# Optimization experiments

Measured on AMD Instinct MI355X. Metric: run time of the kernel, lower is better.

## Reference

```python
import jax, jax.numpy as jnp
import numpy as np

T, C, H, N = 1024, 2048, 32, 64
D_LORA, D_G = 64, 128

def _ln(x, w, b, eps=1e-5):
    m = x.mean(-1, keepdims=True)
    v = ((x - m) ** 2).mean(-1, keepdims=True)
    return (x - m) * jax.lax.rsqrt(v + eps) * w + b

def setup_inputs():
    key = jax.random.key(0)
    ks = iter(jax.random.split(key, 48))
    rn = lambda shape, s=1.0: jax.random.normal(next(ks), shape, dtype=jnp.float32) * s
    return {
        "x": rn((T, C)),
        "x_prev_att": rn((C,)),
        "vk_state": rn((H, N, N), 0.1),
        "x_prev_ffn": rn((C,)),
        "v_first": rn((T, C)),
        "ln1_w": jnp.ones((C,), jnp.float32), "ln1_b": jnp.zeros((C,), jnp.float32),
        "x_r": rn((C,), 0.1), "x_w": rn((C,), 0.1), "x_k": rn((C,), 0.1),
        "x_v": rn((C,), 0.1), "x_a": rn((C,), 0.1), "x_g": rn((C,), 0.1),
        "w0": rn((C,), 0.1), "w1": rn((C, D_LORA), 0.02), "w2": rn((D_LORA, C), 0.02),
        "a0": rn((C,), 0.1), "a1": rn((C, D_LORA), 0.02), "a2": rn((D_LORA, C), 0.02),
        "v0": rn((C,), 0.1), "v1": rn((C, D_LORA), 0.02), "v2": rn((D_LORA, C), 0.02),
        "g1": rn((C, D_G), 0.02), "g2": rn((D_G, C), 0.02),
        "k_k": rn((C,), 0.1), "k_a": rn((C,), 0.1), "r_k": rn((C,), 0.1),
        "R_": rn((C, C), 0.02), "K_": rn((C, C), 0.02),
        "V_": rn((C, C), 0.02), "O_": rn((C, C), 0.02),
        "lnx_w": jnp.ones((C,), jnp.float32), "lnx_b": jnp.zeros((C,), jnp.float32),
        "ln2_w": jnp.ones((C,), jnp.float32), "ln2_b": jnp.zeros((C,), jnp.float32),
        "ffn_x_k": rn((C,), 0.1),
        "ffn_K": rn((C, 4 * C), 0.02), "ffn_V": rn((4 * C, C), 0.02),
    }

def reference(x, x_prev_att, vk_state, x_prev_ffn, v_first, ln1_w, ln1_b,
              x_r, x_w, x_k, x_v, x_a, x_g, w0, w1, w2, a0, a1, a2,
              v0, v1, v2, g1, g2, k_k, k_a, r_k, R_, K_, V_, O_,
              lnx_w, lnx_b, ln2_w, ln2_b, ffn_x_k, ffn_K, ffn_V):
    # ---- TMix: RWKV-7 time mixing (layer_id = 1, so v_first blend is active) ----
    xln = _ln(x, ln1_w, ln1_b)                                  # [T, C]
    dx = jnp.concatenate([x_prev_att[None, :], xln[:-1]], axis=0) - xln  # token shift
    xr, xw, xk, xv, xa, xg = (xln + dx * m for m in (x_r, x_w, x_k, x_v, x_a, x_g))
    r = xr @ R_
    w = jnp.tanh(xw @ w1) @ w2
    k = xk @ K_
    v = xv @ V_
    a = jax.nn.sigmoid(a0 + (xa @ a1) @ a2)
    g = jax.nn.sigmoid(xg @ g1) @ g2
    kk = (k * k_k).reshape(T, H, N)
    kk = kk / jnp.maximum(jnp.linalg.norm(kk, axis=-1, keepdims=True), 1e-12)  # L2 normalize per head
    k = k * (1.0 + (a - 1.0) * k_a)
    v = v + (v_first - v) * jax.nn.sigmoid(v0 + (xv @ v1) @ v2)  # layer_id != 0 path
    w = jnp.exp(-0.606531 * jax.nn.sigmoid(w0 + w))               # per-channel decay in (0,1)
    rh, kh, vh = r.reshape(T, H, N), k.reshape(T, H, N), v.reshape(T, H, N)
    ah, wh = a.reshape(T, H, N), w.reshape(T, H, N)

    def step(state, inp):
        # state: [H, N, N]; generalized delta rule: state*w + state@(-kk)(kk*a)^T + v k^T
        w_t, kk_t, a_t, k_t, v_t, r_t = inp
        ab = jnp.einsum('hi,hj->hij', -kk_t, kk_t * a_t)
        vk = jnp.einsum('hi,hj->hij', v_t, k_t)
        state = state * w_t[:, None, :] + jnp.einsum('hij,hjk->hik', state, ab) + vk
        return state, jnp.einsum('hij,hj->hi', state, r_t)

    vk_state, outs = jax.lax.scan(step, vk_state, (wh, kk, ah, kh, vh, rh))  # outs: [T, H, N]
    # group norm over H groups, eps = 0.00064, affine per-channel
    m = outs.mean(-1, keepdims=True)
    var = ((outs - m) ** 2).mean(-1, keepdims=True)
    gn = ((outs - m) * jax.lax.rsqrt(var + 0.00064)).reshape(T, C) * lnx_w + lnx_b
    bonus = ((r * k * r_k).reshape(T, H, N).sum(-1, keepdims=True) * vh).reshape(T, C)
    x = x + ((gn + bonus) * g) @ O_
    # ---- CMix: gated squared-ReLU MLP ----
    xln2 = _ln(x, ln2_w, ln2_b)
    dx2 = jnp.concatenate([x_prev_ffn[None, :], xln2[:-1]], axis=0) - xln2
    kf = jax.nn.relu((xln2 + dx2 * ffn_x_k) @ ffn_K) ** 2
    x = x + kf @ ffn_V
    return x
```

## Files before the change

### kernel.cpp

```cpp
#include <hip/hip_runtime.h>
#include <hip/hip_bf16.h>


#define T_ 1024
#define C_ 2048
#define H_ 32
#define NH 64

typedef __attribute__((ext_vector_type(8))) short short8v;
typedef __attribute__((ext_vector_type(4))) float f32x4;

__device__ __forceinline__ float bf2f(unsigned short u) {
  union { float f; unsigned int i; } c; c.i = ((unsigned int)u) << 16; return c.f;
}
__device__ __forceinline__ unsigned short f2bf(float f) {
  union { float f; unsigned int i; } c; c.f = f;
  unsigned int x = c.i;
  return (unsigned short)((x + 0x7fffu + ((x >> 16) & 1u)) >> 16);
}
__device__ __forceinline__ float sigm(float x) { return 1.f / (1.f + __expf(-x)); }

__device__ __forceinline__ void load8bf(const unsigned short* p, float* o) {
  union { int4 v; unsigned short u[8]; } c;
  c.v = *(const int4*)p;
#pragma unroll
  for (int i = 0; i < 8; ++i) o[i] = bf2f(c.u[i]);
}
__device__ __forceinline__ void store8bf(unsigned short* p, const float* o) {
  union { int4 v; unsigned short u[8]; } c;
#pragma unroll
  for (int i = 0; i < 8; ++i) c.u[i] = f2bf(o[i]);
  *(int4*)p = c.v;
}
__device__ __forceinline__ void load8f(const float* p, float* o) {
  float4 a = ((const float4*)p)[0], b = ((const float4*)p)[1];
  o[0] = a.x; o[1] = a.y; o[2] = a.z; o[3] = a.w;
  o[4] = b.x; o[5] = b.y; o[6] = b.z; o[7] = b.w;
}
__device__ __forceinline__ void load4f(const float* p, float* o) {
  float4 a = *(const float4*)p;
  o[0] = a.x; o[1] = a.y; o[2] = a.z; o[3] = a.w;
}

#define GLD16(g, l)                                                        \
  __builtin_amdgcn_global_load_lds(                                        \
      (const __attribute__((address_space(1))) void*)(g),                  \
      (__attribute__((address_space(3))) void*)(l), 16, 0, 0)

__global__ __launch_bounds__(256) void ln_kernel(const float* __restrict__ x,
                                                 const float* __restrict__ w,
                                                 const float* __restrict__ b,
                                                 unsigned short* __restrict__ out) {
  int t = blockIdx.x, tid = threadIdx.x;
  const float* xr = x + (size_t)t * C_;
  float v[8];
  load8f(xr + tid * 8, v);
  float s = 0.f, q = 0.f;
#pragma unroll
  for (int i = 0; i < 8; ++i) { s += v[i]; q += v[i] * v[i]; }
  for (int m = 1; m < 64; m <<= 1) { s += __shfl_xor(s, m); q += __shfl_xor(q, m); }
  __shared__ float rs[4], rq[4];
  if ((tid & 63) == 0) { rs[tid >> 6] = s; rq[tid >> 6] = q; }
  __syncthreads();
  s = rs[0] + rs[1] + rs[2] + rs[3];
  q = rq[0] + rq[1] + rq[2] + rq[3];
  float mean = s * (1.f / C_);
  float var = q * (1.f / C_) - mean * mean;
  float rstd = rsqrtf(var + 1e-5f);
  int c = tid * 8;
  float o[8];
#pragma unroll
  for (int i = 0; i < 8; ++i) o[i] = (v[i] - mean) * rstd * w[c + i] + b[c + i];
  store8bf(out + (size_t)t * C_ + c, o);
}

__global__ __launch_bounds__(256) void mix6_kernel(
    const unsigned short* __restrict__ xln, const float* __restrict__ xprev,
    const float* __restrict__ mr, const float* __restrict__ mw,
    const float* __restrict__ mk, const float* __restrict__ mv,
    const float* __restrict__ ma, const float* __restrict__ mg,
    unsigned short* xr, unsigned short* xw, unsigned short* xk,
    unsigned short* xv, unsigned short* xa, unsigned short* xg) {
  int t = blockIdx.x, tid = threadIdx.x, c = tid * 8;
  float cur[8], prv[8];
  load8bf(xln + (size_t)t * C_ + c, cur);
  if (t == 0) load8f(xprev + c, prv);
  else load8bf(xln + (size_t)(t - 1) * C_ + c, prv);
  float cf[8], o[8];
  const float* coefs[6] = {mr, mw, mk, mv, ma, mg};
  unsigned short* outs6[6] = {xr, xw, xk, xv, xa, xg};
#pragma unroll
  for (int a = 0; a < 6; ++a) {
    load8f(coefs[a] + c, cf);
#pragma unroll
    for (int i = 0; i < 8; ++i) o[i] = cur[i] + (prv[i] - cur[i]) * cf[i];
    store8bf(outs6[a] + (size_t)t * C_ + c, o);
  }
}

__global__ __launch_bounds__(256) void mix1_kernel(
    const unsigned short* __restrict__ xln, const float* __restrict__ xprev,
    const float* __restrict__ coef, unsigned short* __restrict__ o) {
  int t = blockIdx.x, tid = threadIdx.x, c = tid * 8;
  float cur[8], prv[8], cf[8], o8[8];
  load8bf(xln + (size_t)t * C_ + c, cur);
  if (t == 0) load8f(xprev + c, prv);
  else load8bf(xln + (size_t)(t - 1) * C_ + c, prv);
  load8f(coef + c, cf);
#pragma unroll
  for (int i = 0; i < 8; ++i) o8[i] = cur[i] + (prv[i] - cur[i]) * cf[i];
  store8bf(o + (size_t)t * C_ + c, o8);
}

__global__ __launch_bounds__(256) void transpose_kernel(
    const float* in0, const float* in1, const float* in2,
    unsigned short* o0, unsigned short* o1, unsigned short* o2,
    int R, int Cc) {
  const float* in = blockIdx.z == 0 ? in0 : (blockIdx.z == 1 ? in1 : in2);
  unsigned short* out = blockIdx.z == 0 ? o0 : (blockIdx.z == 1 ? o1 : o2);
  __shared__ __align__(16) unsigned short tile[64][80];
  int c0 = blockIdx.x * 64, r0 = blockIdx.y * 64;
  int rr = threadIdx.x >> 4, cq = threadIdx.x & 15;
#pragma unroll
  for (int i = 0; i < 4; ++i) {
    int r = rr + i * 16;
    float4 v = *(const float4*)(in + (size_t)(r0 + r) * Cc + c0 + cq * 4);
    tile[cq * 4 + 0][r] = f2bf(v.x);
    tile[cq * 4 + 1][r] = f2bf(v.y);
    tile[cq * 4 + 2][r] = f2bf(v.z);
    tile[cq * 4 + 3][r] = f2bf(v.w);
  }
  __syncthreads();
  int cr = threadIdx.x >> 2, rg = threadIdx.x & 3;
  int4 w0 = *(const int4*)&tile[cr][rg * 16];
  int4 w1 = *(const int4*)&tile[cr][rg * 16 + 8];
  unsigned short* op = out + (size_t)(c0 + cr) * R + r0 + rg * 16;
  *(int4*)op = w0;
  *(int4*)(op + 8) = w1;
}

template <int EPI>
__global__ __launch_bounds__(256) void gemm2_kernel(
    const unsigned short* A0, const unsigned short* A1, const unsigned short* A2,
    const unsigned short* B0, const unsigned short* B1, const unsigned short* B2,
    void* C0, void* C1, void* C2, const float* __restrict__ addsrc,
    int M, int K, int N) {
  int z = blockIdx.z;
  const unsigned short* A = z == 0 ? A0 : (z == 1 ? A1 : A2);
  const unsigned short* Bt = z == 0 ? B0 : (z == 1 ? B1 : B2);
  void* Cout = z == 0 ? C0 : (z == 1 ? C1 : C2);
  __shared__ __align__(16) unsigned short As[128 * 32];
  __shared__ __align__(16) unsigned short Bs[128 * 32];
  const int tid = threadIdx.x, lane = tid & 63, wid = tid >> 6;
  const int bm = blockIdx.y * 128, bn = blockIdx.x * 128;
  const int wr = wid >> 1, wc = wid & 1;
  const int mrow = lane & 15, krow = lane >> 4;
  f32x4 acc[4][4] = {};
  for (int kt = 0; kt < K; kt += 32) {
#pragma unroll
    for (int q = 0; q < 2; ++q) {
      int s = q * 2048 + tid * 8;
      int m = s >> 5, k = s & 31;
      GLD16(A + (size_t)(bm + m) * K + kt + k, &As[s]);
      GLD16(Bt + (size_t)(bn + m) * K + kt + k, &Bs[s]);
    }
    __syncthreads();
    short8v af[4], bfrag[4];
#pragma unroll
    for (int i = 0; i < 4; ++i)
      af[i] = *(const short8v*)&As[(wr * 64 + i * 16 + mrow) * 32 + krow * 8];
#pragma unroll
    for (int j = 0; j < 4; ++j)
      bfrag[j] = *(const short8v*)&Bs[(wc * 64 + j * 16 + mrow) * 32 + krow * 8];
#pragma unroll
    for (int i = 0; i < 4; ++i)
#pragma unroll
      for (int j = 0; j < 4; ++j)
        acc[i][j] = __builtin_amdgcn_mfma_f32_16x16x32_bf16(af[i], bfrag[j], acc[i][j], 0, 0, 0);
    __syncthreads();
  }
#pragma unroll
  for (int i = 0; i < 4; ++i)
#pragma unroll
    for (int j = 0; j < 4; ++j)
#pragma unroll
      for (int e = 0; e < 4; ++e) {
        int grow = bm + wr * 64 + i * 16 + (lane >> 4) * 4 + e;
        int gcol = bn + wc * 64 + j * 16 + (lane & 15);
        size_t off = (size_t)grow * N + gcol;
        float v = acc[i][j][e];
        if constexpr (EPI == 0) ((float*)Cout)[off] = v;
        else if constexpr (EPI == 1) ((float*)Cout)[off] = addsrc[off] + v;
        else { float r = v > 0.f ? v : 0.f; ((unsigned short*)Cout)[off] = f2bf(r * r); }
      }
}

__global__ __launch_bounds__(256) void gemm2ks_kernel(
    const unsigned short* __restrict__ A, const unsigned short* __restrict__ Bt,
    float* __restrict__ P, int M, int KH, int Ktot, int N) {
  int kz = blockIdx.z;
  const size_t kbase = (size_t)kz * KH;
  __shared__ __align__(16) unsigned short As[128 * 32];
  __shared__ __align__(16) unsigned short Bs[128 * 32];
  const int tid = threadIdx.x, lane = tid & 63, wid = tid >> 6;
  const int bm = blockIdx.y * 128, bn = blockIdx.x * 128;
  const int wr = wid >> 1, wc = wid & 1;
  const int mrow = lane & 15, krow = lane >> 4;
  f32x4 acc[4][4] = {};
  for (int kt = 0; kt < KH; kt += 32) {
#pragma unroll
    for (int q = 0; q < 2; ++q) {
      int s = q * 2048 + tid * 8;
      int m = s >> 5, k = s & 31;
      GLD16(A + (size_t)(bm + m) * Ktot + kbase + kt + k, &As[s]);
      GLD16(Bt + (size_t)(bn + m) * Ktot + kbase + kt + k, &Bs[s]);
    }
    __syncthreads();
    short8v af[4], bfrag[4];
#pragma unroll
    for (int i = 0; i < 4; ++i)
      af[i] = *(const short8v*)&As[(wr * 64 + i * 16 + mrow) * 32 + krow * 8];
#pragma unroll
    for (int j = 0; j < 4; ++j)
      bfrag[j] = *(const short8v*)&Bs[(wc * 64 + j * 16 + mrow) * 32 + krow * 8];
#pragma unroll
    for (int i = 0; i < 4; ++i)
#pragma unroll
      for (int j = 0; j < 4; ++j)
        acc[i][j] = __builtin_amdgcn_mfma_f32_16x16x32_bf16(af[i], bfrag[j], acc[i][j], 0, 0, 0);
    __syncthreads();
  }
  float* Pz = P + (size_t)kz * M * N;
#pragma unroll
  for (int i = 0; i < 4; ++i)
#pragma unroll
    for (int j = 0; j < 4; ++j)
#pragma unroll
      for (int e = 0; e < 4; ++e) {
        int grow = bm + wr * 64 + i * 16 + (lane >> 4) * 4 + e;
        int gcol = bn + wc * 64 + j * 16 + (lane & 15);
        Pz[(size_t)grow * N + gcol] = acc[i][j][e];
      }
}

__global__ __launch_bounds__(256) void gemm2ks3_kernel(
    const unsigned short* A0, const unsigned short* A1, const unsigned short* A2,
    const unsigned short* B0, const unsigned short* B1, const unsigned short* B2,
    float* __restrict__ P, int M, int KH, int Ktot, int N) {
  int z = blockIdx.z;
  int batch = z % 3, kz = z / 3;
  const unsigned short* A = batch == 0 ? A0 : (batch == 1 ? A1 : A2);
  const unsigned short* Bt = batch == 0 ? B0 : (batch == 1 ? B1 : B2);
  const size_t kbase = (size_t)kz * KH;
  __shared__ __align__(16) unsigned short As[128 * 32];
  __shared__ __align__(16) unsigned short Bs[128 * 32];
  const int tid = threadIdx.x, lane = tid & 63, wid = tid >> 6;
  const int bm = blockIdx.y * 128, bn = blockIdx.x * 128;
  const int wr = wid >> 1, wc = wid & 1;
  const int mrow = lane & 15, krow = lane >> 4;
  f32x4 acc[4][4] = {};
  for (int kt = 0; kt < KH; kt += 32) {
#pragma unroll
    for (int q = 0; q < 2; ++q) {
      int s = q * 2048 + tid * 8;
      int m = s >> 5, k = s & 31;
      GLD16(A + (size_t)(bm + m) * Ktot + kbase + kt + k, &As[s]);
      GLD16(Bt + (size_t)(bn + m) * Ktot + kbase + kt + k, &Bs[s]);
    }
    __syncthreads();
    short8v af[4], bfrag[4];
#pragma unroll
    for (int i = 0; i < 4; ++i)
      af[i] = *(const short8v*)&As[(wr * 64 + i * 16 + mrow) * 32 + krow * 8];
#pragma unroll
    for (int j = 0; j < 4; ++j)
      bfrag[j] = *(const short8v*)&Bs[(wc * 64 + j * 16 + mrow) * 32 + krow * 8];
#pragma unroll
    for (int i = 0; i < 4; ++i)
#pragma unroll
      for (int j = 0; j < 4; ++j)
        acc[i][j] = __builtin_amdgcn_mfma_f32_16x16x32_bf16(af[i], bfrag[j], acc[i][j], 0, 0, 0);
    __syncthreads();
  }
  float* Pz = P + (size_t)z * M * N;
#pragma unroll
  for (int i = 0; i < 4; ++i)
#pragma unroll
    for (int j = 0; j < 4; ++j)
#pragma unroll
      for (int e = 0; e < 4; ++e) {
        int grow = bm + wr * 64 + i * 16 + (lane >> 4) * 4 + e;
        int gcol = bn + wc * 64 + j * 16 + (lane & 15);
        Pz[(size_t)grow * N + gcol] = acc[i][j][e];
      }
}

__global__ __launch_bounds__(256) void addsk3_kernel(float* __restrict__ q) {
  size_t i = ((size_t)blockIdx.x * 256 + threadIdx.x) * 4;
  float4 a = *(const float4*)(q + i);
  float4 b = *(const float4*)(q + i + 3ull * T_ * C_);
  float4 r;
  r.x = a.x + b.x; r.y = a.y + b.y; r.z = a.z + b.z; r.w = a.w + b.w;
  *(float4*)(q + i) = r;
}

__global__ __launch_bounds__(256) void add5_kernel(
    const float* __restrict__ a, const float* __restrict__ p,
    float* __restrict__ o) {
  size_t i = ((size_t)blockIdx.x * 256 + threadIdx.x) * 4;
  const size_t TC = (size_t)T_ * C_;
  float4 va = *(const float4*)(a + i);
  float4 v0 = *(const float4*)(p + i);
  float4 v1 = *(const float4*)(p + i + TC);
  float4 v2 = *(const float4*)(p + i + 2 * TC);
  float4 v3 = *(const float4*)(p + i + 3 * TC);
  float4 r;
  r.x = va.x + v0.x + v1.x + v2.x + v3.x;
  r.y = va.y + v0.y + v1.y + v2.y + v3.y;
  r.z = va.z + v0.z + v1.z + v2.z + v3.z;
  r.w = va.w + v0.w + v1.w + v2.w + v3.w;
  *(float4*)(o + i) = r;
}

__global__ __launch_bounds__(256) void gemm_ks3_kernel(
    const unsigned short* A0, const unsigned short* A1, const unsigned short* A2,
    const unsigned short* B0, const unsigned short* B1, const unsigned short* B2,
    float* P0, float* P1, float* P2, int K, int N) {
  int mz = blockIdx.z >> 3, kz = blockIdx.z & 7;
  const unsigned short* A = mz == 0 ? A0 : (mz == 1 ? A1 : A2);
  const unsigned short* Bt = mz == 0 ? B0 : (mz == 1 ? B1 : B2);
  float* partial = mz == 0 ? P0 : (mz == 1 ? P1 : P2);
  __shared__ __align__(16) unsigned short As[128 * 32];
  __shared__ __align__(16) unsigned short Bs[64 * 32];
  const int tid = threadIdx.x, lane = tid & 63, wid = tid >> 6;
  const int bn = blockIdx.x * 64, bm = blockIdx.y * 128;
  const int wr = wid >> 1, wc = wid & 1;
  const int mrow = lane & 15, krow = lane >> 4;
  f32x4 acc[4][2] = {};
  for (int kt = kz * 256; kt < kz * 256 + 256; kt += 32) {
#pragma unroll
    for (int q = 0; q < 2; ++q) {
      int s = q * 2048 + tid * 8;
      int m = s >> 5, k = s & 31;
      GLD16(A + (size_t)(bm + m) * K + kt + k, &As[s]);
    }
    {
      int s = tid * 8;
      int n = s >> 5, k = s & 31;
      GLD16(Bt + (size_t)(bn + n) * K + kt + k, &Bs[s]);
    }
    __syncthreads();
    short8v af[4], bfrag[2];
#pragma unroll
    for (int i = 0; i < 4; ++i)
      af[i] = *(const short8v*)&As[(wr * 64 + i * 16 + mrow) * 32 + krow * 8];
#pragma unroll
    for (int j = 0; j < 2; ++j)
      bfrag[j] = *(const short8v*)&Bs[(wc * 32 + j * 16 + mrow) * 32 + krow * 8];
#pragma unroll
    for (int i = 0; i < 4; ++i)
#pragma unroll
      for (int j = 0; j < 2; ++j)
        acc[i][j] = __builtin_amdgcn_mfma_f32_16x16x32_bf16(af[i], bfrag[j], acc[i][j], 0, 0, 0);
    __syncthreads();
  }
#pragma unroll
  for (int i = 0; i < 4; ++i)
#pragma unroll
    for (int j = 0; j < 2; ++j)
#pragma unroll
      for (int e = 0; e < 4; ++e) {
        int row = bm + wr * 64 + i * 16 + (lane >> 4) * 4 + e;
        int col = bn + wc * 32 + j * 16 + (lane & 15);
        partial[((size_t)kz * 1024 + row) * N + col] = acc[i][j][e];
      }
}

__global__ __launch_bounds__(256) void gemm_ks_kernel(
    const unsigned short* __restrict__ A, const unsigned short* __restrict__ Bt,
    float* __restrict__ partial, int K, int N) {
  __shared__ __align__(16) unsigned short As[128 * 32];
  __shared__ __align__(16) unsigned short Bs[64 * 32];
  const int tid = threadIdx.x, lane = tid & 63, wid = tid >> 6;
  const int bn = blockIdx.x * 64, bm = blockIdx.y * 128, kz = blockIdx.z;
  const int wr = wid >> 1, wc = wid & 1;
  const int mrow = lane & 15, krow = lane >> 4;
  f32x4 acc[4][2] = {};
  for (int kt = kz * 256; kt < kz * 256 + 256; kt += 32) {
#pragma unroll
    for (int q = 0; q < 2; ++q) {
      int s = q * 2048 + tid * 8;
      int m = s >> 5, k = s & 31;
      GLD16(A + (size_t)(bm + m) * K + kt + k, &As[s]);
    }
    {
      int s = tid * 8;
      int n = s >> 5, k = s & 31;
      GLD16(Bt + (size_t)(bn + n) * K + kt + k, &Bs[s]);
    }
    __syncthreads();
    short8v af[4], bfrag[2];
#pragma unroll
    for (int i = 0; i < 4; ++i)
      af[i] = *(const short8v*)&As[(wr * 64 + i * 16 + mrow) * 32 + krow * 8];
#pragma unroll
    for (int j = 0; j < 2; ++j)
      bfrag[j] = *(const short8v*)&Bs[(wc * 32 + j * 16 + mrow) * 32 + krow * 8];
#pragma unroll
    for (int i = 0; i < 4; ++i)
#pragma unroll
      for (int j = 0; j < 2; ++j)
        acc[i][j] = __builtin_amdgcn_mfma_f32_16x16x32_bf16(af[i], bfrag[j], acc[i][j], 0, 0, 0);
    __syncthreads();
  }
#pragma unroll
  for (int i = 0; i < 4; ++i)
#pragma unroll
    for (int j = 0; j < 2; ++j)
#pragma unroll
      for (int e = 0; e < 4; ++e) {
        int row = bm + wr * 64 + i * 16 + (lane >> 4) * 4 + e;
        int col = bn + wc * 32 + j * 16 + (lane & 15);
        partial[((size_t)kz * 1024 + row) * N + col] = acc[i][j][e];
      }
}

__global__ __launch_bounds__(128) void lora_combine_kernel(
    const float* __restrict__ pw, const float* __restrict__ pa,
    const float* __restrict__ pv, const float* __restrict__ pg,
    unsigned short* __restrict__ hw, unsigned short* __restrict__ ha,
    unsigned short* __restrict__ hv, unsigned short* __restrict__ hg) {
  int t = blockIdx.x, which = blockIdx.y, tid = threadIdx.x;
  int Nl = (which == 3) ? 128 : 64;
  if (tid >= Nl) return;
  const float* p = which == 0 ? pw : which == 1 ? pa : which == 2 ? pv : pg;
  float s = 0.f;
#pragma unroll
  for (int kz = 0; kz < 8; ++kz) s += p[((size_t)kz * 1024 + t) * Nl + tid];
  float r = which == 0 ? tanhf(s) : (which == 3 ? sigm(s) : s);
  unsigned short* o = which == 0 ? hw : which == 1 ? ha : which == 2 ? hv : hg;
  o[t * Nl + tid] = f2bf(r);
}

__global__ __launch_bounds__(256) void post_kernel(
    const float* __restrict__ k_, const float* __restrict__ vraw,
    const float* __restrict__ r_, const float* __restrict__ wpre,
    const float* __restrict__ apre, const float* __restrict__ vpre,
    const float* __restrict__ vfirst, const float* __restrict__ w0,
    const float* __restrict__ a0, const float* __restrict__ v0_,
    const float* __restrict__ k_k, const float* __restrict__ k_a,
    float* __restrict__ scanin) {
  int t = blockIdx.x, tid = threadIdx.x;
  int c = tid * 8, h = tid >> 3, j = c & 63;
  size_t o = (size_t)t * C_ + c;
  float kv[8], vv[8], rv[8], wv[8], av[8], vp[8], vf[8];
  load8f(k_ + o, kv); load8f(vraw + o, vv); load8f(r_ + o, rv);
  load8f(wpre + o, wv); load8f(apre + o, av); load8f(vpre + o, vp);
  load8f(vfirst + o, vf);
  float ckk[8], cka[8], cw0[8], ca0[8], cv0[8];
  load8f(k_k + c, ckk); load8f(k_a + c, cka); load8f(w0 + c, cw0);
  load8f(a0 + c, ca0); load8f(v0_ + c, cv0);
  float kk[8]; float ss = 0.f;
#pragma unroll
  for (int i = 0; i < 8; ++i) { kk[i] = kv[i] * ckk[i]; ss += kk[i] * kk[i]; }
  ss += __shfl_xor(ss, 1); ss += __shfl_xor(ss, 2); ss += __shfl_xor(ss, 4);
  float rdn = 1.f / fmaxf(sqrtf(ss), 1e-12f);
  float sw[8], skn[8], scc[8], sk2[8], sv[8];
#pragma unroll
  for (int i = 0; i < 8; ++i) {
    float kkn = kk[i] * rdn;
    float a = sigm(ca0[i] + av[i]);
    skn[i] = kkn;
    scc[i] = -kkn * a;
    sk2[i] = kv[i] * (1.f + (a - 1.f) * cka[i]);
    float sg = sigm(cv0[i] + vp[i]);
    sv[i] = vv[i] + (vf[i] - vv[i]) * sg;
    sw[i] = __expf(-0.606531f * sigm(cw0[i] + wv[i]));
  }
  float* bp = scanin + ((size_t)h * T_ + t) * 384 + j;
  ((float4*)(bp + 0))[0]   = make_float4(sw[0], sw[1], sw[2], sw[3]);
  ((float4*)(bp + 4))[0]   = make_float4(sw[4], sw[5], sw[6], sw[7]);
  ((float4*)(bp + 64))[0]  = make_float4(skn[0], skn[1], skn[2], skn[3]);
  ((float4*)(bp + 68))[0]  = make_float4(skn[4], skn[5], skn[6], skn[7]);
  ((float4*)(bp + 128))[0] = make_float4(scc[0], scc[1], scc[2], scc[3]);
  ((float4*)(bp + 132))[0] = make_float4(scc[4], scc[5], scc[6], scc[7]);
  ((float4*)(bp + 192))[0] = make_float4(sk2[0], sk2[1], sk2[2], sk2[3]);
  ((float4*)(bp + 196))[0] = make_float4(sk2[4], sk2[5], sk2[6], sk2[7]);
  ((float4*)(bp + 256))[0] = make_float4(sv[0], sv[1], sv[2], sv[3]);
  ((float4*)(bp + 260))[0] = make_float4(sv[4], sv[5], sv[6], sv[7]);
  ((float4*)(bp + 320))[0] = make_float4(rv[0], rv[1], rv[2], rv[3]);
  ((float4*)(bp + 324))[0] = make_float4(rv[4], rv[5], rv[6], rv[7]);
}

struct SR { float wv[4], nv[4], cv[4], kv[4], rv[4], vvv; };

template <int CTRL>
__device__ __forceinline__ float dppadd(float x) {
  int y = __builtin_amdgcn_update_dpp(0, __float_as_int(x), CTRL, 0xF, 0xF, true);
  return x + __int_as_float(y);
}
__device__ __forceinline__ float red16(float x) {
  x = dppadd<0xB1>(x);
  x = dppadd<0x4E>(x);
  x = dppadd<0x140>(x);
  x = dppadd<0x141>(x);
  return x;
}

__device__ __forceinline__ void loadstep(const float* S, SR& R, int p4, int row) {
  load4f(S + p4, R.wv);
  load4f(S + 64 + p4, R.nv);
  load4f(S + 128 + p4, R.cv);
  load4f(S + 192 + p4, R.kv);
  load4f(S + 320 + p4, R.rv);
  R.vvv = S[256 + row];
}

__device__ __forceinline__ void stepcomp(const SR& R, float* st, int part,
                                         float* __restrict__ ob, size_t oidx) {
  float p0 = fmaf(st[0], R.nv[0], 0.f);
  float p1 = fmaf(st[1], R.nv[1], 0.f);
  p0 = fmaf(st[2], R.nv[2], p0);
  p1 = fmaf(st[3], R.nv[3], p1);
  float sa = red16(p0 + p1);
  float s0 = 0.f, s1 = 0.f;
#pragma unroll
  for (int i = 0; i < 4; ++i) {
    float t = fmaf(st[i], R.wv[i], fmaf(sa, R.cv[i], R.vvv * R.kv[i]));
    st[i] = t;
    if (i & 1) s1 = fmaf(t, R.rv[i], s1);
    else s0 = fmaf(t, R.rv[i], s0);
  }
  float so = red16(s0 + s1);
  if (part == 0) ob[oidx] = so;
}

__global__ __launch_bounds__(64) void scan5_kernel(
    const float* __restrict__ scanin, const float* __restrict__ vk0,
    float* __restrict__ outs) {
  int bid = blockIdx.x;
  int h = (bid & 7) + 8 * ((bid >> 3) & 3);
  int rg = bid >> 5;
  int tid = threadIdx.x;
  int part = tid & 15, row = rg * 4 + (tid >> 4);
  int p4 = part * 4;
  float st[4];
  load4f(vk0 + ((size_t)h * NH + row) * NH + p4, st);
  const float* src = scanin + (size_t)h * T_ * 384;
  float* ob = outs + h * NH + row;
  SR A, B, C, D;
  loadstep(src + 0 * 384, A, p4, row);
  loadstep(src + 1 * 384, B, p4, row);
  loadstep(src + 2 * 384, C, p4, row);
  int s = 0;
  for (; s < T_ - 4; s += 4) {
    const float* sp = src + (size_t)s * 384;
    loadstep(sp + 3 * 384, D, p4, row);
    stepcomp(A, st, part, ob, (size_t)(s + 0) * C_);
    loadstep(sp + 4 * 384, A, p4, row);
    stepcomp(B, st, part, ob, (size_t)(s + 1) * C_);
    loadstep(sp + 5 * 384, B, p4, row);
    stepcomp(C, st, part, ob, (size_t)(s + 2) * C_);
    loadstep(sp + 6 * 384, C, p4, row);
    stepcomp(D, st, part, ob, (size_t)(s + 3) * C_);
  }
  loadstep(src + (size_t)(T_ - 1) * 384, D, p4, row);
  stepcomp(A, st, part, ob, (size_t)(s + 0) * C_);
  stepcomp(B, st, part, ob, (size_t)(s + 1) * C_);
  stepcomp(C, st, part, ob, (size_t)(s + 2) * C_);
  stepcomp(D, st, part, ob, (size_t)(s + 3) * C_);
}

__global__ __launch_bounds__(256) void gnb_kernel(
    const float* __restrict__ outs, const float* __restrict__ scanin,
    const float* __restrict__ g, const float* __restrict__ rk,
    const float* __restrict__ gw, const float* __restrict__ gb,
    unsigned short* __restrict__ attin) {
  int t = blockIdx.x, tid = threadIdx.x;
  int c = tid * 8, h = tid >> 3, j = c & 63;
  float o[8], gv[8], rkv[8];
  load8f(outs + (size_t)t * C_ + c, o);
  load8f(g + (size_t)t * C_ + c, gv);
  load8f(rk + c, rkv);
  size_t sbase = ((size_t)h * T_ + t) * 384 + j;
  float rv[8], k2[8], vv[8];
  load8f(scanin + sbase + 320, rv);
  load8f(scanin + sbase + 192, k2);
  load8f(scanin + sbase + 256, vv);
  float s = 0.f, q = 0.f, bs = 0.f;
#pragma unroll
  for (int i = 0; i < 8; ++i) {
    s += o[i]; q += o[i] * o[i];
    bs += rv[i] * k2[i] * rkv[i];
  }
  s += __shfl_xor(s, 1); s += __shfl_xor(s, 2); s += __shfl_xor(s, 4);
  q += __shfl_xor(q, 1); q += __shfl_xor(q, 2); q += __shfl_xor(q, 4);
  bs += __shfl_xor(bs, 1); bs += __shfl_xor(bs, 2); bs += __shfl_xor(bs, 4);
  float mean = s * (1.f / NH);
  float var = q * (1.f / NH) - mean * mean;
  float rstd = rsqrtf(var + 0.00064f);
  float res[8];
#pragma unroll
  for (int i = 0; i < 8; ++i) {
    float gn = (o[i] - mean) * rstd * gw[c + i] + gb[c + i];
    res[i] = (gn + bs * vv[i]) * gv[i];
  }
  store8bf(attin + (size_t)t * C_ + c, res);
}

extern "C" void kernel_launch(void* const* d_in, const int* in_sizes, int n_in,
                              void* d_out, int out_size, void* d_ws, size_t ws_size,
                              hipStream_t stream) {
  const float* x       = (const float*)d_in[0];
  const float* xprev_a = (const float*)d_in[1];
  const float* vk0     = (const float*)d_in[2];
  const float* xprev_f = (const float*)d_in[3];
  const float* vfirst  = (const float*)d_in[4];
  const float* ln1w = (const float*)d_in[5];
  const float* ln1b = (const float*)d_in[6];
  const float* m_r = (const float*)d_in[7];
  const float* m_w = (const float*)d_in[8];
  const float* m_k = (const float*)d_in[9];
  const float* m_v = (const float*)d_in[10];
  const float* m_a = (const float*)d_in[11];
  const float* m_g = (const float*)d_in[12];
  const float* w0 = (const float*)d_in[13];
  const float* w1 = (const float*)d_in[14];
  const float* w2 = (const float*)d_in[15];
  const float* a0 = (const float*)d_in[16];
  const float* a1 = (const float*)d_in[17];
  const float* a2 = (const float*)d_in[18];
  const float* v0 = (const float*)d_in[19];
  const float* v1 = (const float*)d_in[20];
  const float* v2 = (const float*)d_in[21];
  const float* g1 = (const float*)d_in[22];
  const float* g2 = (const float*)d_in[23];
  const float* k_k = (const float*)d_in[24];
  const float* k_a = (const float*)d_in[25];
  const float* r_k = (const float*)d_in[26];
  const float* R_ = (const float*)d_in[27];
  const float* K_ = (const float*)d_in[28];
  const float* V_ = (const float*)d_in[29];
  const float* O_ = (const float*)d_in[30];
  const float* lnxw = (const float*)d_in[31];
  const float* lnxb = (const float*)d_in[32];
  const float* ln2w = (const float*)d_in[33];
  const float* ln2b = (const float*)d_in[34];
  const float* fxk = (const float*)d_in[35];
  const float* fK = (const float*)d_in[36];
  const float* fV = (const float*)d_in[37];
  float* out = (float*)d_out;

  char* ws = (char*)d_ws;
  const size_t MB = 1ull << 20;
  unsigned short* xln   = (unsigned short*)(ws + 0 * MB);
  unsigned short* attin = (unsigned short*)(ws + 0 * MB);
  unsigned short* xr    = (unsigned short*)(ws + 4 * MB);
  unsigned short* xln2  = (unsigned short*)(ws + 4 * MB);
  unsigned short* xw    = (unsigned short*)(ws + 8 * MB);
  unsigned short* xkf   = (unsigned short*)(ws + 8 * MB);
  unsigned short* xk    = (unsigned short*)(ws + 12 * MB);
  unsigned short* xv    = (unsigned short*)(ws + 16 * MB);
  unsigned short* xa    = (unsigned short*)(ws + 20 * MB);
  unsigned short* xg    = (unsigned short*)(ws + 24 * MB);
  float* qRKV  = (float*)(ws + 28 * MB);
  float* r_buf = (float*)(ws + 28 * MB);
  float* k_buf = (float*)(ws + 36 * MB);
  float* v_buf = (float*)(ws + 44 * MB);
  unsigned short* fVt = (unsigned short*)(ws + 28 * MB);
  float* wpre  = (float*)(ws + 52 * MB);
  float* outsb = (float*)(ws + 52 * MB);
  float* apre  = (float*)(ws + 60 * MB);
  float* x_att = (float*)(ws + 60 * MB);
  float* vpre  = (float*)(ws + 68 * MB);
  float* g_buf = (float*)(ws + 76 * MB);
  float* scanin = (float*)(ws + 84 * MB);
  unsigned short* Rt  = (unsigned short*)(ws + 84 * MB);
  unsigned short* Kt  = (unsigned short*)(ws + 92 * MB);
  unsigned short* Vt  = (unsigned short*)(ws + 100 * MB);
  unsigned short* Ot  = (unsigned short*)(ws + 84 * MB);
  float* qO = (float*)(ws + 92 * MB);
  unsigned short* hffn = (unsigned short*)(ws + 84 * MB);
  unsigned short* fKt  = (unsigned short*)(ws + 100 * MB);
  float* pF = (float*)(ws + 100 * MB);
  unsigned short* w1t = (unsigned short*)(ws + 0);
  unsigned short* a1t = (unsigned short*)(ws + 262144);
  unsigned short* v1t = (unsigned short*)(ws + 524288);
  unsigned short* g1t = (unsigned short*)(ws + 786432);
  unsigned short* hwb = (unsigned short*)(ws + 1310720);
  unsigned short* hab = (unsigned short*)(ws + 1441792);
  unsigned short* hvb = (unsigned short*)(ws + 1572864);
  unsigned short* hgb = (unsigned short*)(ws + 1703936);
  float* pw = (float*)(ws + 2 * MB);
  float* pa = (float*)(ws + 4 * MB);
  float* pv = (float*)(ws + 6 * MB);
  float* pg = (float*)(ws + 8 * MB);
  unsigned short* w2t = (unsigned short*)(ws + 12 * MB);
  unsigned short* a2t = (unsigned short*)(ws + 12 * MB + 262144);
  unsigned short* v2t = (unsigned short*)(ws + 12 * MB + 524288);
  unsigned short* g2t = (unsigned short*)(ws + 12 * MB + 786432);

  ln_kernel<<<T_, 256, 0, stream>>>(x, ln1w, ln1b, xln);
  mix6_kernel<<<T_, 256, 0, stream>>>(xln, xprev_a, m_r, m_w, m_k, m_v, m_a, m_g,
                                      xr, xw, xk, xv, xa, xg);
  transpose_kernel<<<dim3(32, 32, 3), 256, 0, stream>>>(R_, K_, V_, Rt, Kt, Vt, C_, C_);
  gemm2ks3_kernel<<<dim3(16, 8, 6), 256, 0, stream>>>(xr, xk, xv, Rt, Kt, Vt,
                                                      qRKV, T_, 1024, C_, C_);
  addsk3_kernel<<<6144, 256, 0, stream>>>(qRKV);
  transpose_kernel<<<dim3(1, 32, 3), 256, 0, stream>>>(w1, a1, v1, w1t, a1t, v1t, C_, 64);
  transpose_kernel<<<dim3(2, 32, 1), 256, 0, stream>>>(g1, g1, g1, g1t, g1t, g1t, C_, 128);
  gemm_ks3_kernel<<<dim3(1, 8, 24), 256, 0, stream>>>(xw, xa, xv, w1t, a1t, v1t,
                                                      pw, pa, pv, C_, 64);
  gemm_ks_kernel<<<dim3(2, 8, 8), 256, 0, stream>>>(xg, g1t, pg, C_, 128);
  lora_combine_kernel<<<dim3(T_, 4), 128, 0, stream>>>(pw, pa, pv, pg, hwb, hab, hvb, hgb);
  transpose_kernel<<<dim3(32, 1, 3), 256, 0, stream>>>(w2, a2, v2, w2t, a2t, v2t, 64, C_);
  transpose_kernel<<<dim3(32, 2, 1), 256, 0, stream>>>(g2, g2, g2, g2t, g2t, g2t, 128, C_);
  gemm2_kernel<0><<<dim3(16, 8, 3), 256, 0, stream>>>(hwb, hab, hvb, w2t, a2t, v2t,
                                                      wpre, apre, vpre, nullptr, T_, 64, C_);
  gemm2_kernel<0><<<dim3(16, 8, 1), 256, 0, stream>>>(hgb, hgb, hgb, g2t, g2t, g2t,
                                                      g_buf, g_buf, g_buf, nullptr, T_, 128, C_);
  post_kernel<<<T_, 256, 0, stream>>>(k_buf, v_buf, r_buf, wpre, apre, vpre, vfirst,
                                      w0, a0, v0, k_k, k_a, scanin);
  scan5_kernel<<<512, 64, 0, stream>>>(scanin, vk0, outsb);
  gnb_kernel<<<T_, 256, 0, stream>>>(outsb, scanin, g_buf, r_k, lnxw, lnxb, attin);
  transpose_kernel<<<dim3(32, 32, 1), 256, 0, stream>>>(O_, O_, O_, Ot, Ot, Ot, C_, C_);
  transpose_kernel<<<dim3(32, 128, 1), 256, 0, stream>>>(fV, fV, fV, fVt, fVt, fVt, 4 * C_, C_);
  gemm2ks_kernel<<<dim3(16, 8, 4), 256, 0, stream>>>(attin, Ot, qO, T_, 512, C_, C_);
  add5_kernel<<<2048, 256, 0, stream>>>(x, qO, x_att);
  ln_kernel<<<T_, 256, 0, stream>>>(x_att, ln2w, ln2b, xln2);
  mix1_kernel<<<T_, 256, 0, stream>>>(xln2, xprev_f, fxk, xkf);
  transpose_kernel<<<dim3(128, 32, 1), 256, 0, stream>>>(fK, fK, fK, fKt, fKt, fKt, C_, 4 * C_);
  gemm2_kernel<2><<<dim3(64, 8, 1), 256, 0, stream>>>(xkf, xkf, xkf, fKt, fKt, fKt,
                                                      hffn, hffn, hffn, nullptr, T_, C_, 4 * C_);
  gemm2ks_kernel<<<dim3(16, 8, 4), 256, 0, stream>>>(hffn, fVt, pF, T_, 2048, 4 * C_, C_);
  add5_kernel<<<2048, 256, 0, stream>>>(x_att, pF, out);
}
```

Measured before the change: 514.0 us.

## Double-buffer GEMM LDS tiles, fuse split-K reduction into post, store scan inputs in bf16

All GEMM kernels now use two LDS buffers and prefetch the next K tile with global_load_lds while the current tile runs through MFMA. The separate addsk3 kernel that summed split-K partials is removed, and post_kernel adds the two partial halves of r/k/v itself. The scan input buffer is now stored in bf16 instead of fp32, which halves the bytes the scan and gnb kernels read but costs precision in the recurrent state inputs. The wpre/apre/vpre buffers move to new workspace offsets so they do not overlap the qRKV partials that are now read later.

```diff
diff --git a/kernel.cpp b/kernel.cpp
--- a/kernel.cpp
+++ b/kernel.cpp
@@ -26,6 +26,12 @@
 #pragma unroll
   for (int i = 0; i < 8; ++i) o[i] = bf2f(c.u[i]);
 }
+__device__ __forceinline__ void load4bf(const unsigned short* p, float* o) {
+  union { int2 v; unsigned short u[4]; } c;
+  c.v = *(const int2*)p;
+#pragma unroll
+  for (int i = 0; i < 4; ++i) o[i] = bf2f(c.u[i]);
+}
 __device__ __forceinline__ void store8bf(unsigned short* p, const float* o) {
   union { int4 v; unsigned short u[8]; } c;
 #pragma unroll
@@ -36,10 +42,6 @@
   float4 a = ((const float4*)p)[0], b = ((const float4*)p)[1];
   o[0] = a.x; o[1] = a.y; o[2] = a.z; o[3] = a.w;
   o[4] = b.x; o[5] = b.y; o[6] = b.z; o[7] = b.w;
-}
-__device__ __forceinline__ void load4f(const float* p, float* o) {
-  float4 a = *(const float4*)p;
-  o[0] = a.x; o[1] = a.y; o[2] = a.z; o[3] = a.w;
 }
 
 #define GLD16(g, l)                                                        \
@@ -149,35 +151,41 @@
   const unsigned short* A = z == 0 ? A0 : (z == 1 ? A1 : A2);
   const unsigned short* Bt = z == 0 ? B0 : (z == 1 ? B1 : B2);
   void* Cout = z == 0 ? C0 : (z == 1 ? C1 : C2);
-  __shared__ __align__(16) unsigned short As[128 * 32];
-  __shared__ __align__(16) unsigned short Bs[128 * 32];
+  __shared__ __align__(16) unsigned short As[2][128 * 32];
+  __shared__ __align__(16) unsigned short Bs[2][128 * 32];
   const int tid = threadIdx.x, lane = tid & 63, wid = tid >> 6;
   const int bm = blockIdx.y * 128, bn = blockIdx.x * 128;
   const int wr = wid >> 1, wc = wid & 1;
   const int mrow = lane & 15, krow = lane >> 4;
-  f32x4 acc[4][4] = {};
-  for (int kt = 0; kt < K; kt += 32) {
+  auto stage = [&](int buf, int kt) {
 #pragma unroll
     for (int q = 0; q < 2; ++q) {
       int s = q * 2048 + tid * 8;
       int m = s >> 5, k = s & 31;
-      GLD16(A + (size_t)(bm + m) * K + kt + k, &As[s]);
-      GLD16(Bt + (size_t)(bn + m) * K + kt + k, &Bs[s]);
+      GLD16(A + (size_t)(bm + m) * K + kt + k, &As[buf][s]);
+      GLD16(Bt + (size_t)(bn + m) * K + kt + k, &Bs[buf][s]);
     }
-    __syncthreads();
+  };
+  f32x4 acc[4][4] = {};
+  stage(0, 0);
+  __syncthreads();
+  int buf = 0;
+  for (int kt = 0; kt < K; kt += 32) {
+    if (kt + 32 < K) stage(buf ^ 1, kt + 32);
     short8v af[4], bfrag[4];
 #pragma unroll
     for (int i = 0; i < 4; ++i)
-      af[i] = *(const short8v*)&As[(wr * 64 + i * 16 + mrow) * 32 + krow * 8];
+      af[i] = *(const short8v*)&As[buf][(wr * 64 + i * 16 + mrow) * 32 + krow * 8];
 #pragma unroll
     for (int j = 0; j < 4; ++j)
-      bfrag[j] = *(const short8v*)&Bs[(wc * 64 + j * 16 + mrow) * 32 + krow * 8];
+      bfrag[j] = *(const short8v*)&Bs[buf][(wc * 64 + j * 16 + mrow) * 32 + krow * 8];
 #pragma unroll
     for (int i = 0; i < 4; ++i)
 #pragma unroll
       for (int j = 0; j < 4; ++j)
         acc[i][j] = __builtin_amdgcn_mfma_f32_16x16x32_bf16(af[i], bfrag[j], acc[i][j], 0, 0, 0);
     __syncthreads();
+    buf ^= 1;
   }
 #pragma unroll
   for (int i = 0; i < 4; ++i)
@@ -200,35 +208,41 @@
     float* __restrict__ P, int M, int KH, int Ktot, int N) {
   int kz = blockIdx.z;
   const size_t kbase = (size_t)kz * KH;
-  __shared__ __align__(16) unsigned short As[128 * 32];
-  __shared__ __align__(16) unsigned short Bs[128 * 32];
+  __shared__ __align__(16) unsigned short As[2][128 * 32];
+  __shared__ __align__(16) unsigned short Bs[2][128 * 32];
   const int tid = threadIdx.x, lane = tid & 63, wid = tid >> 6;
   const int bm = blockIdx.y * 128, bn = blockIdx.x * 128;
   const int wr = wid >> 1, wc = wid & 1;
   const int mrow = lane & 15, krow = lane >> 4;
-  f32x4 acc[4][4] = {};
-  for (int kt = 0; kt < KH; kt += 32) {
+  auto stage = [&](int buf, int kt) {
 #pragma unroll
     for (int q = 0; q < 2; ++q) {
       int s = q * 2048 + tid * 8;
       int m = s >> 5, k = s & 31;
-      GLD16(A + (size_t)(bm + m) * Ktot + kbase + kt + k, &As[s]);
-      GLD16(Bt + (size_t)(bn + m) * Ktot + kbase + kt + k, &Bs[s]);
+      GLD16(A + (size_t)(bm + m) * Ktot + kbase + kt + k, &As[buf][s]);
+      GLD16(Bt + (size_t)(bn + m) * Ktot + kbase + kt + k, &Bs[buf][s]);
     }
-    __syncthreads();
+  };
+  f32x4 acc[4][4] = {};
+  stage(0, 0);
+  __syncthreads();
+  int buf = 0;
+  for (int kt = 0; kt < KH; kt += 32) {
+    if (kt + 32 < KH) stage(buf ^ 1, kt + 32);
     short8v af[4], bfrag[4];
 #pragma unroll
     for (int i = 0; i < 4; ++i)
-      af[i] = *(const short8v*)&As[(wr * 64 + i * 16 + mrow) * 32 + krow * 8];
+      af[i] = *(const short8v*)&As[buf][(wr * 64 + i * 16 + mrow) * 32 + krow * 8];
 #pragma unroll
     for (int j = 0; j < 4; ++j)
-      bfrag[j] = *(const short8v*)&Bs[(wc * 64 + j * 16 + mrow) * 32 + krow * 8];
+      bfrag[j] = *(const short8v*)&Bs[buf][(wc * 64 + j * 16 + mrow) * 32 + krow * 8];
 #pragma unroll
     for (int i = 0; i < 4; ++i)
 #pragma unroll
       for (int j = 0; j < 4; ++j)
         acc[i][j] = __builtin_amdgcn_mfma_f32_16x16x32_bf16(af[i], bfrag[j], acc[i][j], 0, 0, 0);
     __syncthreads();
+    buf ^= 1;
   }
   float* Pz = P + (size_t)kz * M * N;
 #pragma unroll
@@ -252,35 +266,41 @@
   const unsigned short* A = batch == 0 ? A0 : (batch == 1 ? A1 : A2);
   const unsigned short* Bt = batch == 0 ? B0 : (batch == 1 ? B1 : B2);
   const size_t kbase = (size_t)kz * KH;
-  __shared__ __align__(16) unsigned short As[128 * 32];
-  __shared__ __align__(16) unsigned short Bs[128 * 32];
+  __shared__ __align__(16) unsigned short As[2][128 * 32];
+  __shared__ __align__(16) unsigned short Bs[2][128 * 32];
   const int tid = threadIdx.x, lane = tid & 63, wid = tid >> 6;
   const int bm = blockIdx.y * 128, bn = blockIdx.x * 128;
   const int wr = wid >> 1, wc = wid & 1;
   const int mrow = lane & 15, krow = lane >> 4;
-  f32x4 acc[4][4] = {};
-  for (int kt = 0; kt < KH; kt += 32) {
+  auto stage = [&](int buf, int kt) {
 #pragma unroll
     for (int q = 0; q < 2; ++q) {
       int s = q * 2048 + tid * 8;
       int m = s >> 5, k = s & 31;
-      GLD16(A + (size_t)(bm + m) * Ktot + kbase + kt + k, &As[s]);
-      GLD16(Bt + (size_t)(bn + m) * Ktot + kbase + kt + k, &Bs[s]);
+      GLD16(A + (size_t)(bm + m) * Ktot + kbase + kt + k, &As[buf][s]);
+      GLD16(Bt + (size_t)(bn + m) * Ktot + kbase + kt + k, &Bs[buf][s]);
     }
-    __syncthreads();
+  };
+  f32x4 acc[4][4] = {};
+  stage(0, 0);
+  __syncthreads();
+  int buf = 0;
+  for (int kt = 0; kt < KH; kt += 32) {
+    if (kt + 32 < KH) stage(buf ^ 1, kt + 32);
     short8v af[4], bfrag[4];
 #pragma unroll
     for (int i = 0; i < 4; ++i)
-      af[i] = *(const short8v*)&As[(wr * 64 + i * 16 + mrow) * 32 + krow * 8];
+      af[i] = *(const short8v*)&As[buf][(wr * 64 + i * 16 + mrow) * 32 + krow * 8];
 #pragma unroll
     for (int j = 0; j < 4; ++j)
-      bfrag[j] = *(const short8v*)&Bs[(wc * 64 + j * 16 + mrow) * 32 + krow * 8];
+      bfrag[j] = *(const short8v*)&Bs[buf][(wc * 64 + j * 16 + mrow) * 32 + krow * 8];
 #pragma unroll
     for (int i = 0; i < 4; ++i)
 #pragma unroll
       for (int j = 0; j < 4; ++j)
         acc[i][j] = __builtin_amdgcn_mfma_f32_16x16x32_bf16(af[i], bfrag[j], acc[i][j], 0, 0, 0);
     __syncthreads();
+    buf ^= 1;
   }
   float* Pz = P + (size_t)z * M * N;
 #pragma unroll
@@ -293,15 +313,6 @@
         int gcol = bn + wc * 64 + j * 16 + (lane & 15);
         Pz[(size_t)grow * N + gcol] = acc[i][j][e];
       }
-}
-
-__global__ __launch_bounds__(256) void addsk3_kernel(float* __restrict__ q) {
-  size_t i = ((size_t)blockIdx.x * 256 + threadIdx.x) * 4;
-  float4 a = *(const float4*)(q + i);
-  float4 b = *(const float4*)(q + i + 3ull * T_ * C_);
-  float4 r;
-  r.x = a.x + b.x; r.y = a.y + b.y; r.z = a.z + b.z; r.w = a.w + b.w;
-  *(float4*)(q + i) = r;
 }
 
 __global__ __launch_bounds__(256) void add5_kernel(
@@ -330,39 +341,46 @@
   const unsigned short* A = mz == 0 ? A0 : (mz == 1 ? A1 : A2);
   const unsigned short* Bt = mz == 0 ? B0 : (mz == 1 ? B1 : B2);
   float* partial = mz == 0 ? P0 : (mz == 1 ? P1 : P2);
-  __shared__ __align__(16) unsigned short As[128 * 32];
-  __shared__ __align__(16) unsigned short Bs[64 * 32];
+  __shared__ __align__(16) unsigned short As[2][128 * 32];
+  __shared__ __align__(16) unsigned short Bs[2][64 * 32];
   const int tid = threadIdx.x, lane = tid & 63, wid = tid >> 6;
   const int bn = blockIdx.x * 64, bm = blockIdx.y * 128;
   const int wr = wid >> 1, wc = wid & 1;
   const int mrow = lane & 15, krow = lane >> 4;
-  f32x4 acc[4][2] = {};
-  for (int kt = kz * 256; kt < kz * 256 + 256; kt += 32) {
+  auto stage = [&](int buf, int kt) {
 #pragma unroll
     for (int q = 0; q < 2; ++q) {
       int s = q * 2048 + tid * 8;
       int m = s >> 5, k = s & 31;
-      GLD16(A + (size_t)(bm + m) * K + kt + k, &As[s]);
+      GLD16(A + (size_t)(bm + m) * K + kt + k, &As[buf][s]);
     }
     {
       int s = tid * 8;
       int n = s >> 5, k = s & 31;
-      GLD16(Bt + (size_t)(bn + n) * K + kt + k, &Bs[s]);
+      GLD16(Bt + (size_t)(bn + n) * K + kt + k, &Bs[buf][s]);
     }
-    __syncthreads();
+  };
+  f32x4 acc[4][2] = {};
+  int k0 = kz * 256;
+  stage(0, k0);
+  __syncthreads();
+  int buf = 0;
+  for (int kt = k0; kt < k0 + 256; kt += 32) {
+    if (kt + 32 < k0 + 256) stage(buf ^ 1, kt + 32);
     short8v af[4], bfrag[2];
 #pragma unroll
     for (int i = 0; i < 4; ++i)
-      af[i] = *(const short8v*)&As[(wr * 64 + i * 16 + mrow) * 32 + krow * 8];
+      af[i] = *(const short8v*)&As[buf][(wr * 64 + i * 16 + mrow) * 32 + krow * 8];
 #pragma unroll
     for (int j = 0; j < 2; ++j)
-      bfrag[j] = *(const short8v*)&Bs[(wc * 32 + j * 16 + mrow) * 32 + krow * 8];
+      bfrag[j] = *(const short8v*)&Bs[buf][(wc * 32 + j * 16 + mrow) * 32 + krow * 8];
 #pragma unroll
     for (int i = 0; i < 4; ++i)
 #pragma unroll
       for (int j = 0; j < 2; ++j)
         acc[i][j] = __builtin_amdgcn_mfma_f32_16x16x32_bf16(af[i], bfrag[j], acc[i][j], 0, 0, 0);
     __syncthreads();
+    buf ^= 1;
   }
 #pragma unroll
   for (int i = 0; i < 4; ++i)
@@ -379,39 +397,46 @@
 __global__ __launch_bounds__(256) void gemm_ks_kernel(
     const unsigned short* __restrict__ A, const unsigned short* __restrict__ Bt,
     float* __restrict__ partial, int K, int N) {
-  __shared__ __align__(16) unsigned short As[128 * 32];
-  __shared__ __align__(16) unsigned short Bs[64 * 32];
+  __shared__ __align__(16) unsigned short As[2][128 * 32];
+  __shared__ __align__(16) unsigned short Bs[2][64 * 32];
   const int tid = threadIdx.x, lane = tid & 63, wid = tid >> 6;
   const int bn = blockIdx.x * 64, bm = blockIdx.y * 128, kz = blockIdx.z;
   const int wr = wid >> 1, wc = wid & 1;
   const int mrow = lane & 15, krow = lane >> 4;
-  f32x4 acc[4][2] = {};
-  for (int kt = kz * 256; kt < kz * 256 + 256; kt += 32) {
+  auto stage = [&](int buf, int kt) {
 #pragma unroll
     for (int q = 0; q < 2; ++q) {
       int s = q * 2048 + tid * 8;
       int m = s >> 5, k = s & 31;
-      GLD16(A + (size_t)(bm + m) * K + kt + k, &As[s]);
+      GLD16(A + (size_t)(bm + m) * K + kt + k, &As[buf][s]);
     }
     {
       int s = tid * 8;
       int n = s >> 5, k = s & 31;
-      GLD16(Bt + (size_t)(bn + n) * K + kt + k, &Bs[s]);
+      GLD16(Bt + (size_t)(bn + n) * K + kt + k, &Bs[buf][s]);
     }
-    __syncthreads();
+  };
+  f32x4 acc[4][2] = {};
+  int k0 = kz * 256;
+  stage(0, k0);
+  __syncthreads();
+  int buf = 0;
+  for (int kt = k0; kt < k0 + 256; kt += 32) {
+    if (kt + 32 < k0 + 256) stage(buf ^ 1, kt + 32);
     short8v af[4], bfrag[2];
 #pragma unroll
     for (int i = 0; i < 4; ++i)
-      af[i] = *(const short8v*)&As[(wr * 64 + i * 16 + mrow) * 32 + krow * 8];
+      af[i] = *(const short8v*)&As[buf][(wr * 64 + i * 16 + mrow) * 32 + krow * 8];
 #pragma unroll
     for (int j = 0; j < 2; ++j)
-      bfrag[j] = *(const short8v*)&Bs[(wc * 32 + j * 16 + mrow) * 32 + krow * 8];
+      bfrag[j] = *(const short8v*)&Bs[buf][(wc * 32 + j * 16 + mrow) * 32 + krow * 8];
 #pragma unroll
     for (int i = 0; i < 4; ++i)
 #pragma unroll
       for (int j = 0; j < 2; ++j)
         acc[i][j] = __builtin_amdgcn_mfma_f32_16x16x32_bf16(af[i], bfrag[j], acc[i][j], 0, 0, 0);
     __syncthreads();
+    buf ^= 1;
   }
 #pragma unroll
   for (int i = 0; i < 4; ++i)
@@ -443,18 +468,26 @@
 }
 
 __global__ __launch_bounds__(256) void post_kernel(
-    const float* __restrict__ k_, const float* __restrict__ vraw,
-    const float* __restrict__ r_, const float* __restrict__ wpre,
+    const float* __restrict__ qRKV, const float* __restrict__ wpre,
     const float* __restrict__ apre, const float* __restrict__ vpre,
     const float* __restrict__ vfirst, const float* __restrict__ w0,
     const float* __restrict__ a0, const float* __restrict__ v0_,
     const float* __restrict__ k_k, const float* __restrict__ k_a,
-    float* __restrict__ scanin) {
+    unsigned short* __restrict__ scanin) {
   int t = blockIdx.x, tid = threadIdx.x;
   int c = tid * 8, h = tid >> 3, j = c & 63;
   size_t o = (size_t)t * C_ + c;
-  float kv[8], vv[8], rv[8], wv[8], av[8], vp[8], vf[8];
-  load8f(k_ + o, kv); load8f(vraw + o, vv); load8f(r_ + o, rv);
+  const size_t TC = (size_t)T_ * C_;
+  float rv[8], kv[8], vv[8], t0[8], wv[8], av[8], vp[8], vf[8];
+  load8f(qRKV + o, rv);          load8f(qRKV + 3 * TC + o, t0);
+#pragma unroll
+  for (int i = 0; i < 8; ++i) rv[i] += t0[i];
+  load8f(qRKV + TC + o, kv);     load8f(qRKV + 4 * TC + o, t0);
+#pragma unroll
+  for (int i = 0; i < 8; ++i) kv[i] += t0[i];
+  load8f(qRKV + 2 * TC + o, vv); load8f(qRKV + 5 * TC + o, t0);
+#pragma unroll
+  for (int i = 0; i < 8; ++i) vv[i] += t0[i];
   load8f(wpre + o, wv); load8f(apre + o, av); load8f(vpre + o, vp);
   load8f(vfirst + o, vf);
   float ckk[8], cka[8], cw0[8], ca0[8], cv0[8];
@@ -477,19 +510,13 @@
     sv[i] = vv[i] + (vf[i] - vv[i]) * sg;
     sw[i] = __expf(-0.606531f * sigm(cw0[i] + wv[i]));
   }
-  float* bp = scanin + ((size_t)h * T_ + t) * 384 + j;
-  ((float4*)(bp + 0))[0]   = make_float4(sw[0], sw[1], sw[2], sw[3]);
-  ((float4*)(bp + 4))[0]   = make_float4(sw[4], sw[5], sw[6], sw[7]);
-  ((float4*)(bp + 64))[0]  = make_float4(skn[0], skn[1], skn[2], skn[3]);
-  ((float4*)(bp + 68))[0]  = make_float4(skn[4], skn[5], skn[6], skn[7]);
-  ((float4*)(bp + 128))[0] = make_float4(scc[0], scc[1], scc[2], scc[3]);
-  ((float4*)(bp + 132))[0] = make_float4(scc[4], scc[5], scc[6], scc[7]);
-  ((float4*)(bp + 192))[0] = make_float4(sk2[0], sk2[1], sk2[2], sk2[3]);
-  ((float4*)(bp + 196))[0] = make_float4(sk2[4], sk2[5], sk2[6], sk2[7]);
-  ((float4*)(bp + 256))[0] = make_float4(sv[0], sv[1], sv[2], sv[3]);
-  ((float4*)(bp + 260))[0] = make_float4(sv[4], sv[5], sv[6], sv[7]);
-  ((float4*)(bp + 320))[0] = make_float4(rv[0], rv[1], rv[2], rv[3]);
-  ((float4*)(bp + 324))[0] = make_float4(rv[4], rv[5], rv[6], rv[7]);
+  unsigned short* bp = scanin + ((size_t)h * T_ + t) * 384 + j;
+  store8bf(bp + 0, sw);
+  store8bf(bp + 64, skn);
+  store8bf(bp + 128, scc);
+  store8bf(bp + 192, sk2);
+  store8bf(bp + 256, sv);
+  store8bf(bp + 320, rv);
 }
 
 struct SR { float wv[4], nv[4], cv[4], kv[4], rv[4], vvv; };
@@ -507,13 +534,13 @@
   return x;
 }
 
-__device__ __forceinline__ void loadstep(const float* S, SR& R, int p4, int row) {
-  load4f(S + p4, R.wv);
-  load4f(S + 64 + p4, R.nv);
-  load4f(S + 128 + p4, R.cv);
-  load4f(S + 192 + p4, R.kv);
-  load4f(S + 320 + p4, R.rv);
-  R.vvv = S[256 + row];
+__device__ __forceinline__ void loadstep(const unsigned short* S, SR& R, int p4, int row) {
+  load4bf(S + p4, R.wv);
+  load4bf(S + 64 + p4, R.nv);
+  load4bf(S + 128 + p4, R.cv);
+  load4bf(S + 192 + p4, R.kv);
+  load4bf(S + 320 + p4, R.rv);
+  R.vvv = bf2f(S[256 + row]);
 }
 
 __device__ __forceinline__ void stepcomp(const SR& R, float* st, int part,
@@ -535,8 +562,8 @@
   if (part == 0) ob[oidx] = so;
 }
 
-__global__ __launch_bounds__(64) void scan5_kernel(
-    const float* __restrict__ scanin, const float* __restrict__ vk0,
+__global__ __launch_bounds__(64) void scan7_kernel(
+    const unsigned short* __restrict__ scanin, const float* __restrict__ vk0,
     float* __restrict__ outs) {
   int bid = blockIdx.x;
   int h = (bid & 7) + 8 * ((bid >> 3) & 3);
@@ -545,8 +572,11 @@
   int part = tid & 15, row = rg * 4 + (tid >> 4);
   int p4 = part * 4;
   float st[4];
-  load4f(vk0 + ((size_t)h * NH + row) * NH + p4, st);
-  const float* src = scanin + (size_t)h * T_ * 384;
+  {
+    float4 a = *(const float4*)(vk0 + ((size_t)h * NH + row) * NH + p4);
+    st[0] = a.x; st[1] = a.y; st[2] = a.z; st[3] = a.w;
+  }
+  const unsigned short* src = scanin + (size_t)h * T_ * 384;
   float* ob = outs + h * NH + row;
   SR A, B, C, D;
   loadstep(src + 0 * 384, A, p4, row);
@@ -554,7 +584,7 @@
   loadstep(src + 2 * 384, C, p4, row);
   int s = 0;
   for (; s < T_ - 4; s += 4) {
-    const float* sp = src + (size_t)s * 384;
+    const unsigned short* sp = src + (size_t)s * 384;
     loadstep(sp + 3 * 384, D, p4, row);
     stepcomp(A, st, part, ob, (size_t)(s + 0) * C_);
     loadstep(sp + 4 * 384, A, p4, row);
@@ -572,7 +602,7 @@
 }
 
 __global__ __launch_bounds__(256) void gnb_kernel(
-    const float* __restrict__ outs, const float* __restrict__ scanin,
+    const float* __restrict__ outs, const unsigned short* __restrict__ scanin,
     const float* __restrict__ g, const float* __restrict__ rk,
     const float* __restrict__ gw, const float* __restrict__ gb,
     unsigned short* __restrict__ attin) {
@@ -584,9 +614,9 @@
   load8f(rk + c, rkv);
   size_t sbase = ((size_t)h * T_ + t) * 384 + j;
   float rv[8], k2[8], vv[8];
-  load8f(scanin + sbase + 320, rv);
-  load8f(scanin + sbase + 192, k2);
-  load8f(scanin + sbase + 256, vv);
+  load8bf(scanin + sbase + 320, rv);
+  load8bf(scanin + sbase + 192, k2);
+  load8bf(scanin + sbase + 256, vv);
   float s = 0.f, q = 0.f, bs = 0.f;
 #pragma unroll
   for (int i = 0; i < 8; ++i) {
@@ -664,17 +694,11 @@
   unsigned short* xa    = (unsigned short*)(ws + 20 * MB);
   unsigned short* xg    = (unsigned short*)(ws + 24 * MB);
   float* qRKV  = (float*)(ws + 28 * MB);
-  float* r_buf = (float*)(ws + 28 * MB);
-  float* k_buf = (float*)(ws + 36 * MB);
-  float* v_buf = (float*)(ws + 44 * MB);
   unsigned short* fVt = (unsigned short*)(ws + 28 * MB);
-  float* wpre  = (float*)(ws + 52 * MB);
   float* outsb = (float*)(ws + 52 * MB);
-  float* apre  = (float*)(ws + 60 * MB);
   float* x_att = (float*)(ws + 60 * MB);
-  float* vpre  = (float*)(ws + 68 * MB);
   float* g_buf = (float*)(ws + 76 * MB);
-  float* scanin = (float*)(ws + 84 * MB);
+  unsigned short* scanin = (unsigned short*)(ws + 84 * MB);
   unsigned short* Rt  = (unsigned short*)(ws + 84 * MB);
   unsigned short* Kt  = (unsigned short*)(ws + 92 * MB);
   unsigned short* Vt  = (unsigned short*)(ws + 100 * MB);
@@ -683,6 +707,9 @@
   unsigned short* hffn = (unsigned short*)(ws + 84 * MB);
   unsigned short* fKt  = (unsigned short*)(ws + 100 * MB);
   float* pF = (float*)(ws + 100 * MB);
+  float* wpre  = (float*)(ws + 108 * MB);
+  float* apre  = (float*)(ws + 116 * MB);
+  float* vpre  = (float*)(ws + 124 * MB);
   unsigned short* w1t = (unsigned short*)(ws + 0);
   unsigned short* a1t = (unsigned short*)(ws + 262144);
   unsigned short* v1t = (unsigned short*)(ws + 524288);
@@ -706,7 +733,6 @@
   transpose_kernel<<<dim3(32, 32, 3), 256, 0, stream>>>(R_, K_, V_, Rt, Kt, Vt, C_, C_);
   gemm2ks3_kernel<<<dim3(16, 8, 6), 256, 0, stream>>>(xr, xk, xv, Rt, Kt, Vt,
                                                       qRKV, T_, 1024, C_, C_);
-  addsk3_kernel<<<6144, 256, 0, stream>>>(qRKV);
   transpose_kernel<<<dim3(1, 32, 3), 256, 0, stream>>>(w1, a1, v1, w1t, a1t, v1t, C_, 64);
   transpose_kernel<<<dim3(2, 32, 1), 256, 0, stream>>>(g1, g1, g1, g1t, g1t, g1t, C_, 128);
   gemm_ks3_kernel<<<dim3(1, 8, 24), 256, 0, stream>>>(xw, xa, xv, w1t, a1t, v1t,
@@ -719,9 +745,9 @@
                                                       wpre, apre, vpre, nullptr, T_, 64, C_);
   gemm2_kernel<0><<<dim3(16, 8, 1), 256, 0, stream>>>(hgb, hgb, hgb, g2t, g2t, g2t,
                                                       g_buf, g_buf, g_buf, nullptr, T_, 128, C_);
-  post_kernel<<<T_, 256, 0, stream>>>(k_buf, v_buf, r_buf, wpre, apre, vpre, vfirst,
+  post_kernel<<<T_, 256, 0, stream>>>(qRKV, wpre, apre, vpre, vfirst,
                                       w0, a0, v0, k_k, k_a, scanin);
-  scan5_kernel<<<512, 64, 0, stream>>>(scanin, vk0, outsb);
+  scan7_kernel<<<512, 64, 0, stream>>>(scanin, vk0, outsb);
   gnb_kernel<<<T_, 256, 0, stream>>>(outsb, scanin, g_buf, r_k, lnxw, lnxb, attin);
   transpose_kernel<<<dim3(32, 32, 1), 256, 0, stream>>>(O_, O_, O_, Ot, Ot, Ot, C_, C_);
   transpose_kernel<<<dim3(32, 128, 1), 256, 0, stream>>>(fV, fV, fV, fVt, fVt, fVt, 4 * C_, C_);
```

Result: slower. 546.8 us (+6.4%).
